# Kernel optimization log

Hardware: AMD Instinct MI355X
Metric: run time of the kernel (lower is better)

Reference implementation:

```python
import jax, jax.numpy as jnp
import numpy as np

L, B, P, D, H, DH, KV, M, S, A = 12, 8, 800, 1024, 8, 256, 1, 4096, 50, 32
ROPE_BASE = 10000.0
NEG = -1e30


def _rms(x, w):
    return (x * jax.lax.rsqrt(jnp.mean(x * x, -1, keepdims=True) + 1e-6)) * (1.0 + w)


def _rope(x, cos, sin):
    # x: [B,h,S,DH]; cos/sin: [B,1,S,DH//2]
    x1, x2 = jnp.split(x, 2, axis=-1)
    return jnp.concatenate([x1 * cos - x2 * sin, x2 * cos + x1 * sin], -1)


def setup_inputs() -> dict:
    key = jax.random.key(0)
    ks = iter(jax.random.split(key, 40))
    def nrm(shape, s=0.02):
        return jax.random.normal(next(ks), shape, jnp.float32) * s
    return {
        'prefix_pad_masks': jnp.ones((B, P), jnp.bool_),
        'x_t': jax.random.normal(next(ks), (B, S, A), jnp.float32),
        'timestep': jax.random.uniform(next(ks), (B,), jnp.float32),
        'dt': jnp.full((1,), 0.1, jnp.float32),
        'cache_k': nrm((L, B, KV, P, DH), 1.0),
        'cache_v': nrm((L, B, KV, P, DH), 1.0),
        'w_act_in': nrm((A, D)), 'b_act_in': jnp.zeros((D,), jnp.float32),
        'w_t1': nrm((D, D)), 'b_t1': jnp.zeros((D,), jnp.float32),
        'w_t2': nrm((D, D)), 'b_t2': jnp.zeros((D,), jnp.float32),
        'ln1_w': jnp.zeros((L, D), jnp.float32),
        'ada1_w': nrm((L, D, D)),
        'ln2_w': jnp.zeros((L, D), jnp.float32),
        'wq': nrm((L, D, H * DH)), 'wk': nrm((L, D, KV * DH)),
        'wv': nrm((L, D, KV * DH)), 'wo': nrm((L, H * DH, D)),
        'wg': nrm((L, D, M)), 'wu': nrm((L, D, M)), 'wd': nrm((L, M, D)),
        'lnf_w': jnp.zeros((D,), jnp.float32), 'adaf_w': nrm((D, D)),
        'w_act_out': nrm((D, A)), 'b_act_out': jnp.zeros((A,), jnp.float32),
    }


def reference(prefix_pad_masks, x_t, timestep, dt, cache_k, cache_v,
              w_act_in, b_act_in, w_t1, b_t1, w_t2, b_t2,
              ln1_w, ada1_w, ln2_w, wq, wk, wv, wo, wg, wu, wd,
              lnf_w, adaf_w, w_act_out, b_act_out):
    b, s, _ = x_t.shape
    p = prefix_pad_masks.shape[1]
    # --- embed_suffix: action projection + sinusoidal time -> MLP -> adaRMS cond ---
    suffix = x_t @ w_act_in + b_act_in                              # [B,S,D]
    half = D // 2
    freqs = jnp.exp(-jnp.log(jnp.float32(10000.0)) * jnp.arange(half, dtype=jnp.float32) / half)
    ang = timestep[:, None] * freqs[None, :]
    temb = jnp.concatenate([jnp.sin(ang), jnp.cos(ang)], -1)        # [B,D]
    cond = jax.nn.silu(temb @ w_t1 + b_t1) @ w_t2 + b_t2            # adarms_cond [B,D]
    # --- prefix-suffix 2D attention mask (make_att_2d_masks_trt) ---
    suffix_pad = jnp.ones((b, s), jnp.int32)
    suffix_att = jnp.concatenate([jnp.ones((b, 1), jnp.int32), jnp.zeros((b, s - 1), jnp.int32)], 1)
    cums = jnp.cumsum(suffix_att, 1)
    att2d = cums[:, None, :] <= cums[:, :, None]
    pad2d = (suffix_pad[:, None, :] * suffix_pad[:, :, None]).astype(bool)
    pre2d = jnp.broadcast_to(prefix_pad_masks[:, None, :], (b, s, p))
    full = jnp.concatenate([pre2d, att2d & pad2d], 2)               # [B,S,P+S]
    bias = jnp.where(full, 0.0, NEG)[:, None, :, :].astype(jnp.float32)
    # --- position ids: prefix offset + suffix cumsum - 1 ---
    offs = jnp.sum(prefix_pad_masks.astype(jnp.int32), -1)[:, None]
    pos = offs + jnp.cumsum(suffix_pad, 1) - 1                      # [B,S]
    inv = 1.0 / (ROPE_BASE ** (jnp.arange(0, DH, 2, dtype=jnp.float32) / DH))
    rang = pos[..., None].astype(jnp.float32) * inv                 # [B,S,DH/2]
    cos = jnp.cos(rang)[:, None]
    sin = jnp.sin(rang)[:, None]
    # --- gemma expert (eager attention over KV cache + suffix) ---
    h = suffix * jnp.sqrt(jnp.float32(D))
    def layer(hc, xs):
        l1, a1, l2, Wq, Wk, Wv, Wo, Wg, Wu, Wd, ck, cv = xs
        x = _rms(hc, l1) * (1.0 + (cond @ a1)[:, None, :])
        q = (x @ Wq).reshape(b, s, H, DH).transpose(0, 2, 1, 3)
        k = (x @ Wk).reshape(b, s, KV, DH).transpose(0, 2, 1, 3)
        v = (x @ Wv).reshape(b, s, KV, DH).transpose(0, 2, 1, 3)
        q = _rope(q, cos, sin)
        k = _rope(k, cos, sin)
        kf = jnp.repeat(jnp.concatenate([ck, k], 2), H // KV, 1)    # [B,H,P+S,DH]
        vf = jnp.repeat(jnp.concatenate([cv, v], 2), H // KV, 1)
        sc = jnp.einsum('bhsd,bhtd->bhst', q, kf) / jnp.sqrt(jnp.float32(DH)) + bias
        at = jax.nn.softmax(sc, -1)
        o = jnp.einsum('bhst,bhtd->bhsd', at, vf).transpose(0, 2, 1, 3).reshape(b, s, H * DH)
        hc = hc + o @ Wo
        x2 = _rms(hc, l2)
        hc = hc + (jax.nn.gelu(x2 @ Wg, approximate=True) * (x2 @ Wu)) @ Wd
        return hc, None
    h, _ = jax.lax.scan(layer, h, (ln1_w, ada1_w, ln2_w, wq, wk, wv, wo, wg, wu, wd, cache_k, cache_v))
    hf = _rms(h, lnf_w) * (1.0 + (cond @ adaf_w)[:, None, :])
    v_t = hf[:, -S:].astype(jnp.float32) @ w_act_out + b_act_out    # action_out_proj
    return x_t + dt.reshape(1, 1, 1) * v_t                          # Euler step
```

## Files before the change

kernel.cpp:

```cpp
#include <hip/hip_runtime.h>
#include <hip/hip_bf16.h>
#include <math.h>

#define NLAYER 12
#define NB 8
#define NP 800
#define ND 1024
#define NH 8
#define NDH 256
#define NM 4096
#define NS 50
#define NA 32
#define NKEYS 850
#define KPAD 896

typedef unsigned short ushort_t;
typedef unsigned int u32;
using f32x4  = __attribute__((ext_vector_type(4))) float;
using short8 = __attribute__((ext_vector_type(8))) short;

__device__ __forceinline__ u32 pack_bf2(float lo, float hi) {
  u32 a = __float_as_uint(lo);
  u32 b = __float_as_uint(hi);
  a += 0x7fffu + ((a >> 16) & 1u);
  b += 0x7fffu + ((b >> 16) & 1u);
  return (a >> 16) | (b & 0xffff0000u);
}
__device__ __forceinline__ ushort_t bf1(float x) {
  u32 a = __float_as_uint(x);
  a += 0x7fffu + ((a >> 16) & 1u);
  return (ushort_t)(a >> 16);
}
__device__ __forceinline__ float ubf(ushort_t h) {
  return __uint_as_float(((u32)h) << 16);
}
__device__ __forceinline__ void async_cp16(const void* g, const void* l) {
  __builtin_amdgcn_global_load_lds(
      (const __attribute__((address_space(1))) u32*)g,
      (__attribute__((address_space(3))) u32*)l, 16, 0, 0);
}


__global__ void cvt_copy_kernel(const float* __restrict__ src, ushort_t* __restrict__ dst, long n) {
  long i = ((long)blockIdx.x * 256 + threadIdx.x) * 8;
  if (i >= n) return;
  const float4* s4 = reinterpret_cast<const float4*>(src + i);
  float4 a = s4[0], b = s4[1];
  *reinterpret_cast<uint4*>(dst + i) =
      make_uint4(pack_bf2(a.x, a.y), pack_bf2(a.z, a.w),
                 pack_bf2(b.x, b.y), pack_bf2(b.z, b.w));
}

template<int MODE>
__global__ __launch_bounds__(256) void transpose_cvt(
    const float* __restrict__ src, long sz, ushort_t* __restrict__ dst, long dz,
    int R, int C, int ldd, int halfOff) {
  __shared__ float Ls[64][65];
  const float* s = src + (long)blockIdx.z * sz;
  ushort_t* d    = dst + (long)blockIdx.z * dz;
  int c0 = blockIdx.x * 64, r0 = blockIdx.y * 64;
  int t = threadIdx.x;
  int rr = t >> 4;
  int cc = (t & 15) * 4;
#pragma unroll
  for (int j = 0; j < 4; ++j) {
    int rl = rr + j * 16;
    int r = r0 + rl;
    float4 v = make_float4(0.f, 0.f, 0.f, 0.f);
    if (r < R) v = *reinterpret_cast<const float4*>(s + (long)r * C + c0 + cc);
    Ls[rl][cc] = v.x; Ls[rl][cc+1] = v.y; Ls[rl][cc+2] = v.z; Ls[rl][cc+3] = v.w;
  }
  __syncthreads();
  int dr = t >> 2;
  int rc = (t & 3) * 16;
  int cg = c0 + dr;
  long orow;
  if (MODE == 0) orow = cg;
  else           orow = ((long)(cg >> 5) << 6) + (cg & 31) + halfOff;
  ushort_t* drow = d + orow * ldd + r0 + rc;
#pragma unroll
  for (int i = 0; i < 16; i += 2) {
    int sr = r0 + rc + i;
    if (sr < R) {
      u32 p = pack_bf2(Ls[rc + i][dr], Ls[rc + i + 1][dr]);
      *reinterpret_cast<u32*>(drow + i) = p;
    }
  }
}


__global__ void temb_kernel(const float* __restrict__ ts, float* __restrict__ temb) {
  int idx = blockIdx.x * 256 + threadIdx.x;
  if (idx >= NB * ND) return;
  int b = idx >> 10, d = idx & 1023;
  int i = d & 511;
  float f = __expf(-logf(10000.f) * (float)i / 512.f);
  float ang = ts[b] * f;
  temb[idx] = (d < 512) ? sinf(ang) : cosf(ang);
}

__global__ void suffix_kernel(const float* __restrict__ x_t, const float* __restrict__ w,
                              const float* __restrict__ bias, float* __restrict__ h) {
  int m = blockIdx.x;
  __shared__ float xs[NA];
  if (threadIdx.x < NA) xs[threadIdx.x] = x_t[m * NA + threadIdx.x];
  __syncthreads();
  for (int n = threadIdx.x; n < ND; n += 256) {
    float acc = bias[n];
#pragma unroll
    for (int k = 0; k < NA; ++k) acc += xs[k] * w[k * ND + n];
    h[m * ND + n] = acc * 32.0f;
  }
}

__global__ void rope_table_kernel(float* __restrict__ cosT, float* __restrict__ sinT) {
  int idx = blockIdx.x * 256 + threadIdx.x;
  if (idx >= NS * 128) return;
  int s = idx >> 7, i = idx & 127;
  float inv = __expf(-(float)(2 * i) / 256.f * logf(10000.f));
  float ang = (float)(NP + s) * inv;
  cosT[idx] = cosf(ang);
  sinT[idx] = sinf(ang);
}

__global__ void rope3_kernel(const ushort_t* __restrict__ qkv0, const ushort_t* __restrict__ qkv1,
                             const float* __restrict__ cosT, const float* __restrict__ sinT,
                             ushort_t* __restrict__ qT, ushort_t* __restrict__ k_new,
                             ushort_t* __restrict__ vT_l) {
  int idx = blockIdx.x * 256 + threadIdx.x;
  if (idx >= 400 * 10 * 128) return;
  int i = idx & 127;
  int rest = idx >> 7;
  int hh = rest % 10;
  int m = rest / 10;
  int b = m / NS, s = m % NS;
  if (hh == 9) {
    int d = i;
    long base = (long)m * 2560 + 2304;
    float v0 = ubf(qkv0[base + d])       + ubf(qkv1[base + d]);
    float v1 = ubf(qkv0[base + d + 128]) + ubf(qkv1[base + d + 128]);
    vT_l[((long)(b * 256 + d)) * KPAD + NP + s]       = bf1(v0);
    vT_l[((long)(b * 256 + d + 128)) * KPAD + NP + s] = bf1(v1);
    return;
  }
  float c = cosT[s * 128 + i], sn = sinT[s * 128 + i];
  if (hh < NH) {
    long base = (long)m * 2560 + hh * 256;
    float x1 = ubf(qkv0[base + i])       + ubf(qkv1[base + i]);
    float x2 = ubf(qkv0[base + 128 + i]) + ubf(qkv1[base + 128 + i]);
    ushort_t* dst = qT + (((long)(b * NH + hh) * NS + s) * 256);
    dst[i]       = bf1(x1 * c - x2 * sn);
    dst[128 + i] = bf1(x2 * c + x1 * sn);
  } else {
    long base = (long)m * 2560 + 2048;
    float x1 = ubf(qkv0[base + i])       + ubf(qkv1[base + i]);
    float x2 = ubf(qkv0[base + 128 + i]) + ubf(qkv1[base + 128 + i]);
    ushort_t* dst = k_new + (long)m * 256;
    dst[i]       = bf1(x1 * c - x2 * sn);
    dst[128 + i] = bf1(x2 * c + x1 * sn);
  }
}

template<bool BFOUT>
__global__ void rms_kernel(const float* __restrict__ hin, const float* __restrict__ w,
                           const float* __restrict__ ada, void* __restrict__ outv) {
  int m = blockIdx.x;
  int b = m / NS;
  int d0 = threadIdx.x * 4;
  float4 v = *reinterpret_cast<const float4*>(hin + (long)m * ND + d0);
  float ss = v.x*v.x + v.y*v.y + v.z*v.z + v.w*v.w;
#pragma unroll
  for (int off = 32; off > 0; off >>= 1) ss += __shfl_down(ss, off);
  __shared__ float red[4];
  int lane = threadIdx.x & 63, wid = threadIdx.x >> 6;
  if (lane == 0) red[wid] = ss;
  __syncthreads();
  float tot = red[0] + red[1] + red[2] + red[3];
  float r = rsqrtf(tot * (1.f / ND) + 1e-6f);
  float4 wv = *reinterpret_cast<const float4*>(w + d0);
  float4 o;
  o.x = v.x * r * (1.f + wv.x);
  o.y = v.y * r * (1.f + wv.y);
  o.z = v.z * r * (1.f + wv.z);
  o.w = v.w * r * (1.f + wv.w);
  if (ada) {
    float4 av = *reinterpret_cast<const float4*>(ada + (long)b * ND + d0);
    o.x *= (1.f + av.x); o.y *= (1.f + av.y); o.z *= (1.f + av.z); o.w *= (1.f + av.w);
  }
  if (BFOUT) {
    *reinterpret_cast<uint2*>((ushort_t*)outv + (long)m * ND + d0) =
        make_uint2(pack_bf2(o.x, o.y), pack_bf2(o.z, o.w));
  } else {
    *reinterpret_cast<float4*>((float*)outv + (long)m * ND + d0) = o;
  }
}

__global__ void softmax_kernel(const float* __restrict__ sc, ushort_t* __restrict__ P) {
  int row = blockIdx.x;
  const float* p = sc + (long)row * KPAD;
  ushort_t* o = P + (long)row * KPAD;
  __shared__ float e[NKEYS];
  __shared__ float red[4];
  int lane = threadIdx.x & 63, wid = threadIdx.x >> 6;
  float mx = -1e30f;
  for (int t = threadIdx.x; t < NKEYS; t += 256) { float v = p[t]; e[t] = v; mx = fmaxf(mx, v); }
#pragma unroll
  for (int off = 32; off > 0; off >>= 1) mx = fmaxf(mx, __shfl_down(mx, off));
  if (lane == 0) red[wid] = mx;
  __syncthreads();
  mx = fmaxf(fmaxf(red[0], red[1]), fmaxf(red[2], red[3]));
  __syncthreads();
  float sum = 0.f;
  for (int t = threadIdx.x; t < NKEYS; t += 256) {
    float v = __expf(e[t] - mx);
    e[t] = v;
    sum += v;
  }
#pragma unroll
  for (int off = 32; off > 0; off >>= 1) sum += __shfl_down(sum, off);
  if (lane == 0) red[wid] = sum;
  __syncthreads();
  float inv = 1.f / (red[0] + red[1] + red[2] + red[3]);
  for (int t = threadIdx.x; t < KPAD; t += 256)
    o[t] = (t < NKEYS) ? bf1(e[t] * inv) : (ushort_t)0;
}

__global__ void final_kernel(const float* __restrict__ hf, const float* __restrict__ w,
                             const float* __restrict__ bias, const float* __restrict__ x_t,
                             const float* __restrict__ dt, float* __restrict__ out) {
  int m = blockIdx.x;
  int a = threadIdx.x & 31;
  int kg = threadIdx.x >> 5;
  float acc = 0.f;
  for (int k = kg; k < ND; k += 8) acc += hf[(long)m * ND + k] * w[k * NA + a];
  __shared__ float red[256];
  red[threadIdx.x] = acc;
  __syncthreads();
  if (threadIdx.x < NA) {
    float s = 0.f;
#pragma unroll
    for (int g = 0; g < 8; ++g) s += red[g * 32 + a];
    out[m * NA + a] = x_t[m * NA + a] + dt[0] * (s + bias[a]);
  }
}

template<int EPI, bool SPL, bool SPLITK>
__global__ __launch_bounds__(256) void gemm64(
    const ushort_t* __restrict__ A, long az,
    const ushort_t* __restrict__ B1, long b1z,
    const ushort_t* __restrict__ B2, long b2z, int nsplit, int nlim2,
    void* __restrict__ Cv, long cz,
    int M, int N, int K, int lda, int ldb, int ldc,
    float scale, int kpb, const ushort_t* __restrict__ zpad) {
  int z = blockIdx.z;
  int chunk = 0;
  int kbeg = 0, kend = K;
  if (SPLITK) { chunk = z; kbeg = z * kpb; kend = kbeg + kpb; z = 0; }
  const ushort_t* Ab  = A  + (long)z * az;
  const ushort_t* B1b = B1 + (long)z * b1z;
  const ushort_t* B2b = SPL ? (B2 + (long)z * b2z) : nullptr;

  const int m0 = blockIdx.x * 64;
  const int n0 = blockIdx.y * 64;
  const int tid = threadIdx.x;
  const int lane = tid & 63;
  const int wbase = tid & 192;
  const int wid = wbase >> 6;
  const int wm = (wid >> 1) * 32;
  const int wn = (wid & 1) * 32;
  const int l15 = lane & 15;
  const int l4  = lane >> 4;

  __shared__ ushort_t As[2][64 * 64];
  __shared__ ushort_t Bs[2][64 * 64];

  f32x4 acc[2][2] = {};

  const int ci0 = wbase + lane;
  const int row0 = ci0 >> 3;
  const int kc0 = (ci0 & 7) << 3;
  const int ci1 = 256 + ci0;
  const int row1 = ci1 >> 3;
  const int kc1 = (ci1 & 7) << 3;
  int gra0 = m0 + row0; if (gra0 > M - 1) gra0 = M - 1;
  int gra1 = m0 + row1; if (gra1 > M - 1) gra1 = M - 1;
  const int n_0 = n0 + row0;
  const int n_1 = n0 + row1;

  auto stage = [&](int buf, int k0) {
    async_cp16(Ab + (long)gra0 * lda + k0 + kc0, (const char*)As[buf] + (wbase + lane) * 16 - lane * 16 + lane * 16);
    const ushort_t* gp0;
    const ushort_t* gp1;
    if (SPL) {
      gp0 = (n_0 < nsplit) ? B1b + (long)n_0 * ldb + k0 + kc0
          : (n_0 < nlim2)  ? B2b + (long)(n_0 - nsplit) * ldb + k0 + kc0
                           : zpad + kc0;
      gp1 = (n_1 < nsplit) ? B1b + (long)n_1 * ldb + k0 + kc1
          : (n_1 < nlim2)  ? B2b + (long)(n_1 - nsplit) * ldb + k0 + kc1
                           : zpad + kc1;
    } else {
      gp0 = B1b + (long)n_0 * ldb + k0 + kc0;
      gp1 = B1b + (long)n_1 * ldb + k0 + kc1;
    }
    async_cp16(gp0, (const char*)Bs[buf] + ci0 * 16);
    async_cp16(Ab + (long)gra1 * lda + k0 + kc1, (const char*)As[buf] + ci1 * 16);
    async_cp16(gp1, (const char*)Bs[buf] + ci1 * 16);
  };

  const int nt = (kend - kbeg) >> 6;
  stage(0, kbeg);
  __syncthreads();
  int cur = 0;
  for (int t = 0; t < nt; ++t) {
    if (t + 1 < nt) stage(cur ^ 1, kbeg + (t + 1) * 64);
    const ushort_t* Ac = As[cur];
    const ushort_t* Bc = Bs[cur];
#pragma unroll
    for (int ks = 0; ks < 2; ++ks) {
      short8 af[2], bf[2];
#pragma unroll
      for (int mi = 0; mi < 2; ++mi)
        af[mi] = *reinterpret_cast<const short8*>(&Ac[(wm + mi * 16 + l15) * 64 + ks * 32 + l4 * 8]);
#pragma unroll
      for (int ni = 0; ni < 2; ++ni)
        bf[ni] = *reinterpret_cast<const short8*>(&Bc[(wn + ni * 16 + l15) * 64 + ks * 32 + l4 * 8]);
#pragma unroll
      for (int mi = 0; mi < 2; ++mi)
#pragma unroll
        for (int ni = 0; ni < 2; ++ni)
          acc[mi][ni] = __builtin_amdgcn_mfma_f32_16x16x32_bf16(af[mi], bf[ni], acc[mi][ni], 0, 0, 0);
    }
    __syncthreads();
    cur ^= 1;
  }

#pragma unroll
  for (int mi = 0; mi < 2; ++mi) {
#pragma unroll
    for (int ni = 0; ni < 2; ++ni) {
      int col = n0 + wn + ni * 16 + l15;
      int rb  = m0 + wm + mi * 16 + l4 * 4;
      if (col >= N) continue;
#pragma unroll
      for (int r = 0; r < 4; ++r) {
        int row = rb + r;
        if (row >= M) continue;
        float v = acc[mi][ni][r];
        if (EPI == 0) {
          ((float*)Cv)[(long)z * cz + (long)row * ldc + col] = v * scale;
        } else if (EPI == 3) {
          atomicAdd(&((float*)Cv)[(long)row * ldc + col], v);
        } else if (EPI == 4) {
          int hh = row / NS;
          int s  = row - hh * NS;
          ((ushort_t*)Cv)[((long)(blockIdx.z * NS + s)) * 2048 + hh * 256 + col] = bf1(v);
        } else if (EPI == 5) {
          long slab = SPLITK ? (long)chunk : (long)z;
          ((ushort_t*)Cv)[slab * cz + (long)row * ldc + col] = bf1(v);
        }
      }
    }
  }
}

__global__ __launch_bounds__(256) void gemm64G(
    const ushort_t* __restrict__ A, const ushort_t* __restrict__ B,
    ushort_t* __restrict__ C, int M, int K, int lda, int ldb, int ldc) {
  const int m0 = blockIdx.x * 64;
  const int n0 = blockIdx.y * 64;
  const int tid = threadIdx.x;
  const int lane = tid & 63;
  const int wbase = tid & 192;
  const int wid = wbase >> 6;
  const int l15 = lane & 15;
  const int l4  = lane >> 4;

  __shared__ ushort_t As[2][64 * 64];
  __shared__ ushort_t Bs[2][64 * 64];

  f32x4 acc[4] = {};

  const int ci0 = wbase + lane;
  const int row0 = ci0 >> 3;
  const int kc0 = (ci0 & 7) << 3;
  const int ci1 = 256 + ci0;
  const int row1 = ci1 >> 3;
  const int kc1 = (ci1 & 7) << 3;
  int gra0 = m0 + row0; if (gra0 > M - 1) gra0 = M - 1;
  int gra1 = m0 + row1; if (gra1 > M - 1) gra1 = M - 1;

  auto stage = [&](int buf, int k0) {
    async_cp16(A + (long)gra0 * lda + k0 + kc0, (const char*)As[buf] + ci0 * 16);
    async_cp16(B + (long)(n0 + row0) * ldb + k0 + kc0, (const char*)Bs[buf] + ci0 * 16);
    async_cp16(A + (long)gra1 * lda + k0 + kc1, (const char*)As[buf] + ci1 * 16);
    async_cp16(B + (long)(n0 + row1) * ldb + k0 + kc1, (const char*)Bs[buf] + ci1 * 16);
  };

  const int nt = K >> 6;
  stage(0, 0);
  __syncthreads();
  int cur = 0;
  for (int t = 0; t < nt; ++t) {
    if (t + 1 < nt) stage(cur ^ 1, (t + 1) * 64);
    const ushort_t* Ac = As[cur];
    const ushort_t* Bc = Bs[cur];
#pragma unroll
    for (int ks = 0; ks < 2; ++ks) {
      short8 af = *reinterpret_cast<const short8*>(&Ac[(wid * 16 + l15) * 64 + ks * 32 + l4 * 8]);
#pragma unroll
      for (int ni = 0; ni < 4; ++ni) {
        short8 bf = *reinterpret_cast<const short8*>(&Bc[(ni * 16 + l15) * 64 + ks * 32 + l4 * 8]);
        acc[ni] = __builtin_amdgcn_mfma_f32_16x16x32_bf16(af, bf, acc[ni], 0, 0, 0);
      }
    }
    __syncthreads();
    cur ^= 1;
  }

#pragma unroll
  for (int ni = 0; ni < 2; ++ni) {
    int col = (n0 >> 1) + ni * 16 + l15;
    int rb  = m0 + wid * 16 + l4 * 4;
#pragma unroll
    for (int r = 0; r < 4; ++r) {
      int row = rb + r;
      if (row >= M) continue;
      float g = acc[ni][r];
      float u = acc[ni + 2][r];
      float inner = 0.7978845608028654f * (g + 0.044715f * g * g * g);
      float t = 0.5f * g * (1.f + tanhf(inner));
      C[(long)row * ldc + col] = bf1(t * u);
    }
  }
}

template<int EPI>
__global__ __launch_bounds__(256)
void gemm_f32_kernel(const float* __restrict__ A,
                     const float* __restrict__ B1,
                     float* __restrict__ C,
                     int M, int N, int K, int lda, int ldb, int ldc,
                     const float* __restrict__ bias) {
  const int m0 = blockIdx.x * 64;
  const int n0 = blockIdx.y * 64;
// ... 134 lines not shown
        int kga = k0 + kg * 16 + kk;
        float v0 = Bb[(long)kga * ldb + gn];
        float v1 = Bb[(long)(kga + 1) * ldb + gn];
        pk[kk >> 1] = pack_bf2(v0, v1);
      }
      *reinterpret_cast<uint4*>(&Bs[n][kg * 16])     = make_uint4(pk[0],pk[1],pk[2],pk[3]);
      *reinterpret_cast<uint4*>(&Bs[n][kg * 16 + 8]) = make_uint4(pk[4],pk[5],pk[6],pk[7]);
    }
    __syncthreads();
#pragma unroll
    for (int ks = 0; ks < 2; ++ks) {
      short8 af[2], bfr[2];
#pragma unroll
      for (int mi = 0; mi < 2; ++mi)
        af[mi] = *reinterpret_cast<const short8*>(&As[wm + mi*16 + l15][ks*32 + l4*8]);
#pragma unroll
      for (int ni = 0; ni < 2; ++ni)
        bfr[ni] = *reinterpret_cast<const short8*>(&Bs[wn + ni*16 + l15][ks*32 + l4*8]);
#pragma unroll
      for (int mi = 0; mi < 2; ++mi)
#pragma unroll
        for (int ni = 0; ni < 2; ++ni)
          acc[mi][ni] = __builtin_amdgcn_mfma_f32_16x16x32_bf16(af[mi], bfr[ni], acc[mi][ni], 0, 0, 0);
    }
    __syncthreads();
  }

#pragma unroll
  for (int mi = 0; mi < 2; ++mi) {
#pragma unroll
    for (int ni = 0; ni < 2; ++ni) {
      int col = n0 + wn + ni * 16 + l15;
      int rb  = m0 + wm + mi * 16 + l4 * 4;
#pragma unroll
      for (int r = 0; r < 4; ++r) {
        int row = rb + r;
        if (row < M && col < N)
          atomicAdd(&Cb[(long)row * ldc + col], acc[mi][ni][r]);
      }
    }
  }
}

extern "C" void kernel_launch(void* const* d_in, const int* in_sizes, int n_in,
                              void* d_out, int out_size, void* d_ws, size_t ws_size,
                              hipStream_t stream) {
  (void)in_sizes; (void)n_in; (void)out_size; (void)ws_size;
  const float* x_t      = (const float*)d_in[1];
  const float* tstep    = (const float*)d_in[2];
  const float* dtp      = (const float*)d_in[3];
  const float* cache_k  = (const float*)d_in[4];
  const float* cache_v  = (const float*)d_in[5];
  const float* w_act_in = (const float*)d_in[6];
  const float* b_act_in = (const float*)d_in[7];
  const float* w_t1     = (const float*)d_in[8];
  const float* b_t1     = (const float*)d_in[9];
  const float* w_t2     = (const float*)d_in[10];
  const float* b_t2     = (const float*)d_in[11];
  const float* ln1_w    = (const float*)d_in[12];
  const float* ada1_w   = (const float*)d_in[13];
  const float* ln2_w    = (const float*)d_in[14];
  const float* wq       = (const float*)d_in[15];
  const float* wk       = (const float*)d_in[16];
  const float* wv       = (const float*)d_in[17];
  const float* wo       = (const float*)d_in[18];
  const float* wg       = (const float*)d_in[19];
  const float* wu       = (const float*)d_in[20];
  const float* wd       = (const float*)d_in[21];
  const float* lnf_w    = (const float*)d_in[22];
  const float* adaf_w   = (const float*)d_in[23];
  const float* wao      = (const float*)d_in[24];
  const float* bao      = (const float*)d_in[25];
  float* outp = (float*)d_out;

  char* p = (char*)d_ws;
  auto alloc = [&](size_t bytes) { char* r = p; p += (bytes + 255) & ~(size_t)255; return r; };

  ushort_t* wqkvT  = (ushort_t*)alloc((size_t)12 * 2560 * 1024 * 2);
  ushort_t* woT    = (ushort_t*)alloc((size_t)12 * 1024 * 2048 * 2);
  ushort_t* wguT   = (ushort_t*)alloc((size_t)12 * 8192 * 1024 * 2);
  ushort_t* wdT    = (ushort_t*)alloc((size_t)12 * 1024 * 4096 * 2);
  ushort_t* kcache = (ushort_t*)alloc((size_t)12 * 8 * NP * 256 * 2);
  ushort_t* vT     = (ushort_t*)alloc((size_t)12 * 8 * 256 * KPAD * 2);
  ushort_t* qkvp   = (ushort_t*)alloc((size_t)2 * 400 * 2560 * 2);
  ushort_t* qT     = (ushort_t*)alloc((size_t)8 * 400 * 256 * 2);
  ushort_t* k_new  = (ushort_t*)alloc((size_t)400 * 256 * 2);
  float*    sc     = (float*)alloc((size_t)8 * 400 * KPAD * 4);
  ushort_t* P      = (ushort_t*)alloc((size_t)8 * 400 * KPAD * 2);
  ushort_t* o_buf  = (ushort_t*)alloc((size_t)400 * 2048 * 2);
  ushort_t* t_buf  = (ushort_t*)alloc((size_t)400 * 4096 * 2);
  ushort_t* x_buf  = (ushort_t*)alloc((size_t)400 * 1024 * 2);
  float*    h_buf  = (float*)alloc((size_t)400 * 1024 * 4);
  float*    hf     = (float*)alloc((size_t)400 * 1024 * 4);
  float*    temb   = (float*)alloc(8 * 1024 * 4);
  float*    tmp    = (float*)alloc(8 * 1024 * 4);
  float*    cond   = (float*)alloc(8 * 1024 * 4);
  float*    ada_all= (float*)alloc((size_t)12 * 8 * 1024 * 4);
  float*    adaf_o = (float*)alloc(8 * 1024 * 4);
  float*    cosT   = (float*)alloc(NS * 128 * 4);
  float*    sinT   = (float*)alloc(NS * 128 * 4);
  ushort_t* zpad   = (ushort_t*)alloc(512 * 2);

  hipMemsetAsync(zpad, 0, 512 * 2, stream);
  hipMemsetAsync(ada_all, 0, ((size_t)12 * 8 * 1024 + 8 * 1024) * 4, stream);

  {
    long n = (long)12 * 8 * NP * 256;
    cvt_copy_kernel<<<(int)((n / 8 + 255) / 256), 256, 0, stream>>>(cache_k, kcache, n);
  }
  transpose_cvt<0><<<dim3(32, 16, 12), 256, 0, stream>>>(wq, (long)1024 * 2048, wqkvT, (long)2560 * 1024, 1024, 2048, 1024, 0);
  transpose_cvt<0><<<dim3(4, 16, 12), 256, 0, stream>>>(wk, (long)1024 * 256, wqkvT + (long)2048 * 1024, (long)2560 * 1024, 1024, 256, 1024, 0);
  transpose_cvt<0><<<dim3(4, 16, 12), 256, 0, stream>>>(wv, (long)1024 * 256, wqkvT + (long)2304 * 1024, (long)2560 * 1024, 1024, 256, 1024, 0);
  transpose_cvt<0><<<dim3(16, 32, 12), 256, 0, stream>>>(wo, (long)2048 * 1024, woT, (long)1024 * 2048, 2048, 1024, 2048, 0);
  transpose_cvt<1><<<dim3(64, 16, 12), 256, 0, stream>>>(wg, (long)1024 * 4096, wguT, (long)8192 * 1024, 1024, 4096, 1024, 0);
  transpose_cvt<1><<<dim3(64, 16, 12), 256, 0, stream>>>(wu, (long)1024 * 4096, wguT, (long)8192 * 1024, 1024, 4096, 1024, 32);
  transpose_cvt<0><<<dim3(16, 64, 12), 256, 0, stream>>>(wd, (long)4096 * 1024, wdT, (long)1024 * 4096, 4096, 1024, 4096, 0);
  transpose_cvt<0><<<dim3(4, 13, 96), 256, 0, stream>>>(cache_v, (long)NP * 256, vT, (long)256 * KPAD, NP, 256, KPAD, 0);

  temb_kernel<<<32, 256, 0, stream>>>(tstep, temb);
  suffix_kernel<<<400, 256, 0, stream>>>(x_t, w_act_in, b_act_in, h_buf);
  rope_table_kernel<<<25, 256, 0, stream>>>(cosT, sinT);
  gemm_f32_kernel<2><<<dim3(1, 16, 1), 256, 0, stream>>>(temb, w_t1, tmp, NB, ND, ND, ND, ND, ND, b_t1);
  gemm_f32_kernel<1><<<dim3(1, 16, 1), 256, 0, stream>>>(tmp, w_t2, cond, NB, ND, ND, ND, ND, ND, b_t2);
  gemm_f32sk<<<dim3(1, 16, 48), 256, 0, stream>>>(cond, ada1_w, (long)ND * ND, ada_all, (long)NB * ND, NB, ND, ND, ND, ND, ND, 4);
  gemm_f32sk<<<dim3(1, 16, 4), 256, 0, stream>>>(cond, adaf_w, 0, adaf_o, 0, NB, ND, ND, ND, ND, ND, 4);

  for (int l = 0; l < NLAYER; ++l) {
    rms_kernel<true><<<400, 256, 0, stream>>>(h_buf, ln1_w + (long)l * ND, ada_all + (long)l * NB * ND, x_buf);
    gemm64<5, false, true><<<dim3(7, 40, 2), 256, 0, stream>>>(
        x_buf, 0, wqkvT + (long)l * 2560 * 1024, 0, nullptr, 0, 0, 0,
        qkvp, (long)400 * 2560, 400, 2560, 1024, 1024, 1024, 2560, 1.f, 512, zpad);
    rope3_kernel<<<2000, 256, 0, stream>>>(qkvp, qkvp + (long)400 * 2560, cosT, sinT,
                                           qT, k_new, vT + (long)l * 8 * 256 * KPAD);
    gemm64<0, true, false><<<dim3(7, 14, 8), 256, 0, stream>>>(
        qT, (long)400 * 256,
        kcache + (long)l * 8 * NP * 256, (long)NP * 256,
        k_new, (long)NS * 256, NP, NKEYS,
        sc, (long)400 * KPAD, 400, KPAD, 256, 256, 256, KPAD, 0.0625f, 0, zpad);
    softmax_kernel<<<3200, 256, 0, stream>>>(sc, P);
    gemm64<4, false, false><<<dim3(7, 4, 8), 256, 0, stream>>>(
        P, (long)400 * KPAD,
        vT + (long)l * 8 * 256 * KPAD, (long)256 * KPAD, nullptr, 0, 0, 0,
        o_buf, 0, 400, 256, KPAD, KPAD, KPAD, 2048, 1.f, 0, zpad);
    gemm64<3, false, true><<<dim3(7, 16, 4), 256, 0, stream>>>(
        o_buf, 0, woT + (long)l * 1024 * 2048, 0, nullptr, 0, 0, 0,
        h_buf, 0, 400, 1024, 2048, 2048, 2048, 1024, 1.f, 512, zpad);
    rms_kernel<true><<<400, 256, 0, stream>>>(h_buf, ln2_w + (long)l * ND, nullptr, x_buf);
    gemm64G<<<dim3(7, 128, 1), 256, 0, stream>>>(
        x_buf, wguT + (long)l * 8192 * 1024, t_buf, 400, 1024, 1024, 1024, 4096);
    gemm64<3, false, true><<<dim3(7, 16, 4), 256, 0, stream>>>(
        t_buf, 0, wdT + (long)l * 1024 * 4096, 0, nullptr, 0, 0, 0,
        h_buf, 0, 400, 1024, 4096, 4096, 4096, 1024, 1.f, 1024, zpad);
  }

  rms_kernel<false><<<400, 256, 0, stream>>>(h_buf, lnf_w, adaf_o, hf);
  final_kernel<<<400, 256, 0, stream>>>(hf, wao, bao, x_t, dtp, outp);
}
```

Measured before the change: 2.049 ms.

## Fuse RoPE into QKV GEMM and replace attention with split-K flash kernel

Interleaves the rotary halves in the Q/K weight and K-cache layouts so the QKV GEMM epilogue can apply RoPE with a lane shuffle. This removes the split-K partial buffer and the separate rope kernel. Attention's score GEMM, softmax and PV GEMM are replaced by a flash-style kernel that splits keys into 128-key chunks, followed by a combine kernel that merges the per-chunk max and sum. The score and probability matrices no longer go through global memory, at the cost of fp32 partial outputs per chunk and an extra combine pass. The QKV GEMM also drops its split-K, which halves its grid parallelism.

```diff
diff --git a/kernel.cpp b/kernel.cpp
--- a/kernel.cpp
+++ b/kernel.cpp
@@ -13,6 +13,7 @@
 #define NA 32
 #define NKEYS 850
 #define KPAD 896
+#define CH 128
 
 typedef unsigned short ushort_t;
 typedef unsigned int u32;
@@ -41,14 +42,18 @@
 }
 
 
-__global__ void cvt_copy_kernel(const float* __restrict__ src, ushort_t* __restrict__ dst, long n) {
-  long i = ((long)blockIdx.x * 256 + threadIdx.x) * 8;
-  if (i >= n) return;
-  const float4* s4 = reinterpret_cast<const float4*>(src + i);
-  float4 a = s4[0], b = s4[1];
-  *reinterpret_cast<uint4*>(dst + i) =
-      make_uint4(pack_bf2(a.x, a.y), pack_bf2(a.z, a.w),
-                 pack_bf2(b.x, b.y), pack_bf2(b.z, b.w));
+__global__ void cvt_permute_kernel(const float* __restrict__ src, ushort_t* __restrict__ dst, long nrows) {
+  long idx = (long)blockIdx.x * 256 + threadIdx.x;
+  long row = idx >> 5;
+  int t = (int)(idx & 31);
+  if (row >= nrows) return;
+  const float* s = src + row * 256 + t * 4;
+  float4 lo = *reinterpret_cast<const float4*>(s);
+  float4 hi = *reinterpret_cast<const float4*>(s + 128);
+  ushort_t* d = dst + row * 256 + t * 8;
+  *reinterpret_cast<uint4*>(d) =
+      make_uint4(pack_bf2(lo.x, hi.x), pack_bf2(lo.y, hi.y),
+                 pack_bf2(lo.z, hi.z), pack_bf2(lo.w, hi.w));
 }
 
 template<int MODE>
@@ -75,8 +80,9 @@
   int rc = (t & 3) * 16;
   int cg = c0 + dr;
   long orow;
-  if (MODE == 0) orow = cg;
-  else           orow = ((long)(cg >> 5) << 6) + (cg & 31) + halfOff;
+  if (MODE == 0)      orow = cg;
+  else if (MODE == 1) orow = ((long)(cg >> 5) << 6) + (cg & 31) + halfOff;
+  else                orow = (long)(cg & ~255) + ((cg & 127) << 1) + ((cg >> 7) & 1);
   ushort_t* drow = d + orow * ldd + r0 + rc;
 #pragma unroll
   for (int i = 0; i < 16; i += 2) {
@@ -121,44 +127,6 @@
   float ang = (float)(NP + s) * inv;
   cosT[idx] = cosf(ang);
   sinT[idx] = sinf(ang);
-}
-
-__global__ void rope3_kernel(const ushort_t* __restrict__ qkv0, const ushort_t* __restrict__ qkv1,
-                             const float* __restrict__ cosT, const float* __restrict__ sinT,
-                             ushort_t* __restrict__ qT, ushort_t* __restrict__ k_new,
-                             ushort_t* __restrict__ vT_l) {
-  int idx = blockIdx.x * 256 + threadIdx.x;
-  if (idx >= 400 * 10 * 128) return;
-  int i = idx & 127;
-  int rest = idx >> 7;
-  int hh = rest % 10;
-  int m = rest / 10;
-  int b = m / NS, s = m % NS;
-  if (hh == 9) {
-    int d = i;
-    long base = (long)m * 2560 + 2304;
-    float v0 = ubf(qkv0[base + d])       + ubf(qkv1[base + d]);
-    float v1 = ubf(qkv0[base + d + 128]) + ubf(qkv1[base + d + 128]);
-    vT_l[((long)(b * 256 + d)) * KPAD + NP + s]       = bf1(v0);
-    vT_l[((long)(b * 256 + d + 128)) * KPAD + NP + s] = bf1(v1);
-    return;
-  }
-  float c = cosT[s * 128 + i], sn = sinT[s * 128 + i];
-  if (hh < NH) {
-    long base = (long)m * 2560 + hh * 256;
-    float x1 = ubf(qkv0[base + i])       + ubf(qkv1[base + i]);
-    float x2 = ubf(qkv0[base + 128 + i]) + ubf(qkv1[base + 128 + i]);
-    ushort_t* dst = qT + (((long)(b * NH + hh) * NS + s) * 256);
-    dst[i]       = bf1(x1 * c - x2 * sn);
-    dst[128 + i] = bf1(x2 * c + x1 * sn);
-  } else {
-    long base = (long)m * 2560 + 2048;
-    float x1 = ubf(qkv0[base + i])       + ubf(qkv1[base + i]);
-    float x2 = ubf(qkv0[base + 128 + i]) + ubf(qkv1[base + 128 + i]);
-    ushort_t* dst = k_new + (long)m * 256;
-    dst[i]       = bf1(x1 * c - x2 * sn);
-    dst[128 + i] = bf1(x2 * c + x1 * sn);
-  }
 }
 
 template<bool BFOUT>
@@ -195,36 +163,6 @@
   }
 }
 
-__global__ void softmax_kernel(const float* __restrict__ sc, ushort_t* __restrict__ P) {
-  int row = blockIdx.x;
-  const float* p = sc + (long)row * KPAD;
-  ushort_t* o = P + (long)row * KPAD;
-  __shared__ float e[NKEYS];
-  __shared__ float red[4];
-  int lane = threadIdx.x & 63, wid = threadIdx.x >> 6;
-  float mx = -1e30f;
-  for (int t = threadIdx.x; t < NKEYS; t += 256) { float v = p[t]; e[t] = v; mx = fmaxf(mx, v); }
-#pragma unroll
-  for (int off = 32; off > 0; off >>= 1) mx = fmaxf(mx, __shfl_down(mx, off));
-  if (lane == 0) red[wid] = mx;
-  __syncthreads();
-  mx = fmaxf(fmaxf(red[0], red[1]), fmaxf(red[2], red[3]));
-  __syncthreads();
-  float sum = 0.f;
-  for (int t = threadIdx.x; t < NKEYS; t += 256) {
-    float v = __expf(e[t] - mx);
-    e[t] = v;
-    sum += v;
-  }
-#pragma unroll
-  for (int off = 32; off > 0; off >>= 1) sum += __shfl_down(sum, off);
-  if (lane == 0) red[wid] = sum;
-  __syncthreads();
-  float inv = 1.f / (red[0] + red[1] + red[2] + red[3]);
-  for (int t = threadIdx.x; t < KPAD; t += 256)
-    o[t] = (t < NKEYS) ? bf1(e[t] * inv) : (ushort_t)0;
-}
-
 __global__ void final_kernel(const float* __restrict__ hf, const float* __restrict__ w,
                              const float* __restrict__ bias, const float* __restrict__ x_t,
                              const float* __restrict__ dt, float* __restrict__ out) {
@@ -244,21 +182,13 @@
   }
 }
 
-template<int EPI, bool SPL, bool SPLITK>
-__global__ __launch_bounds__(256) void gemm64(
-    const ushort_t* __restrict__ A, long az,
-    const ushort_t* __restrict__ B1, long b1z,
-    const ushort_t* __restrict__ B2, long b2z, int nsplit, int nlim2,
-    void* __restrict__ Cv, long cz,
-    int M, int N, int K, int lda, int ldb, int ldc,
-    float scale, int kpb, const ushort_t* __restrict__ zpad) {
-  int z = blockIdx.z;
-  int chunk = 0;
-  int kbeg = 0, kend = K;
-  if (SPLITK) { chunk = z; kbeg = z * kpb; kend = kbeg + kpb; z = 0; }
-  const ushort_t* Ab  = A  + (long)z * az;
-  const ushort_t* B1b = B1 + (long)z * b1z;
-  const ushort_t* B2b = SPL ? (B2 + (long)z * b2z) : nullptr;
+__global__ __launch_bounds__(256) void gemm64acc(
+    const ushort_t* __restrict__ A,
+    const ushort_t* __restrict__ B,
+    float* __restrict__ C,
+    int M, int N, int K, int lda, int ldb, int ldc, int kpb) {
+  const int kbeg = blockIdx.z * kpb;
+  const int kend = kbeg + kpb;
 
   const int m0 = blockIdx.x * 64;
   const int n0 = blockIdx.y * 64;
@@ -288,23 +218,10 @@
   const int n_1 = n0 + row1;
 
   auto stage = [&](int buf, int k0) {
-    async_cp16(Ab + (long)gra0 * lda + k0 + kc0, (const char*)As[buf] + (wbase + lane) * 16 - lane * 16 + lane * 16);
-    const ushort_t* gp0;
-    const ushort_t* gp1;
-    if (SPL) {
-      gp0 = (n_0 < nsplit) ? B1b + (long)n_0 * ldb + k0 + kc0
-          : (n_0 < nlim2)  ? B2b + (long)(n_0 - nsplit) * ldb + k0 + kc0
-                           : zpad + kc0;
-      gp1 = (n_1 < nsplit) ? B1b + (long)n_1 * ldb + k0 + kc1
-          : (n_1 < nlim2)  ? B2b + (long)(n_1 - nsplit) * ldb + k0 + kc1
-                           : zpad + kc1;
-    } else {
-      gp0 = B1b + (long)n_0 * ldb + k0 + kc0;
-      gp1 = B1b + (long)n_1 * ldb + k0 + kc1;
-    }
-    async_cp16(gp0, (const char*)Bs[buf] + ci0 * 16);
-    async_cp16(Ab + (long)gra1 * lda + k0 + kc1, (const char*)As[buf] + ci1 * 16);
-    async_cp16(gp1, (const char*)Bs[buf] + ci1 * 16);
+    async_cp16(A + (long)gra0 * lda + k0 + kc0, (const char*)As[buf] + ci0 * 16);
+    async_cp16(B + (long)n_0 * ldb + k0 + kc0, (const char*)Bs[buf] + ci0 * 16);
+    async_cp16(A + (long)gra1 * lda + k0 + kc1, (const char*)As[buf] + ci1 * 16);
+    async_cp16(B + (long)n_1 * ldb + k0 + kc1, (const char*)Bs[buf] + ci1 * 16);
   };
 
   const int nt = (kend - kbeg) >> 6;
@@ -345,21 +262,324 @@
       for (int r = 0; r < 4; ++r) {
         int row = rb + r;
         if (row >= M) continue;
+        atomicAdd(&C[(long)row * ldc + col], acc[mi][ni][r]);
+      }
+    }
+  }
+}
+
+__global__ __launch_bounds__(256) void gemm64rope(
+    const ushort_t* __restrict__ A,
+    const ushort_t* __restrict__ B,
+    const float* __restrict__ cosT, const float* __restrict__ sinT,
+    ushort_t* __restrict__ qTo, ushort_t* __restrict__ k_new,
+    ushort_t* __restrict__ vT_l) {
+  const int M = 400, K = 1024, lda = 1024, ldb = 1024;
+  const int m0 = blockIdx.x * 64;
+  const int n0 = blockIdx.y * 64;
+  const int tid = threadIdx.x;
+  const int lane = tid & 63;
+  const int wbase = tid & 192;
+  const int wid = wbase >> 6;
+  const int wm = (wid >> 1) * 32;
+  const int wn = (wid & 1) * 32;
+  const int l15 = lane & 15;
+  const int l4  = lane >> 4;
+
+  __shared__ ushort_t As[2][64 * 64];
+  __shared__ ushort_t Bs[2][64 * 64];
+
+  f32x4 acc[2][2] = {};
+
+  const int ci0 = wbase + lane;
+  const int row0 = ci0 >> 3;
+  const int kc0 = (ci0 & 7) << 3;
+  const int ci1 = 256 + ci0;
+  const int row1 = ci1 >> 3;
+  const int kc1 = (ci1 & 7) << 3;
+  int gra0 = m0 + row0; if (gra0 > M - 1) gra0 = M - 1;
+  int gra1 = m0 + row1; if (gra1 > M - 1) gra1 = M - 1;
+  const int n_0 = n0 + row0;
+  const int n_1 = n0 + row1;
+
+  auto stage = [&](int buf, int k0) {
+    async_cp16(A + (long)gra0 * lda + k0 + kc0, (const char*)As[buf] + ci0 * 16);
+    async_cp16(B + (long)n_0 * ldb + k0 + kc0, (const char*)Bs[buf] + ci0 * 16);
+    async_cp16(A + (long)gra1 * lda + k0 + kc1, (const char*)As[buf] + ci1 * 16);
+    async_cp16(B + (long)n_1 * ldb + k0 + kc1, (const char*)Bs[buf] + ci1 * 16);
+  };
+
+  stage(0, 0);
+  __syncthreads();
+  int cur = 0;
+  for (int t = 0; t < 16; ++t) {
+    if (t + 1 < 16) stage(cur ^ 1, (t + 1) * 64);
+    const ushort_t* Ac = As[cur];
+    const ushort_t* Bc = Bs[cur];
+#pragma unroll
+    for (int ks = 0; ks < 2; ++ks) {
+      short8 af[2], bf[2];
+#pragma unroll
+      for (int mi = 0; mi < 2; ++mi)
+        af[mi] = *reinterpret_cast<const short8*>(&Ac[(wm + mi * 16 + l15) * 64 + ks * 32 + l4 * 8]);
+#pragma unroll
+      for (int ni = 0; ni < 2; ++ni)
+        bf[ni] = *reinterpret_cast<const short8*>(&Bc[(wn + ni * 16 + l15) * 64 + ks * 32 + l4 * 8]);
+#pragma unroll
+      for (int mi = 0; mi < 2; ++mi)
+#pragma unroll
+        for (int ni = 0; ni < 2; ++ni)
+          acc[mi][ni] = __builtin_amdgcn_mfma_f32_16x16x32_bf16(af[mi], bf[ni], acc[mi][ni], 0, 0, 0);
+    }
+    __syncthreads();
+    cur ^= 1;
+  }
+
+#pragma unroll
+  for (int mi = 0; mi < 2; ++mi) {
+#pragma unroll
+    for (int ni = 0; ni < 2; ++ni) {
+      int col = n0 + wn + ni * 16 + l15;
+      int rb  = m0 + wm + mi * 16 + l4 * 4;
+      float pv[4];
+#pragma unroll
+      for (int r = 0; r < 4; ++r) pv[r] = __shfl_xor(acc[mi][ni][r], 1);
+#pragma unroll
+      for (int r = 0; r < 4; ++r) {
+        int row = rb + r;
+        if (row >= 400) continue;
+        int b = row / NS, s = row - b * NS;
         float v = acc[mi][ni][r];
-        if (EPI == 0) {
-          ((float*)Cv)[(long)z * cz + (long)row * ldc + col] = v * scale;
-        } else if (EPI == 3) {
-          atomicAdd(&((float*)Cv)[(long)row * ldc + col], v);
-        } else if (EPI == 4) {
-          int hh = row / NS;
-          int s  = row - hh * NS;
-          ((ushort_t*)Cv)[((long)(blockIdx.z * NS + s)) * 2048 + hh * 256 + col] = bf1(v);
-        } else if (EPI == 5) {
-          long slab = SPLITK ? (long)chunk : (long)z;
-          ((ushort_t*)Cv)[slab * cz + (long)row * ldc + col] = bf1(v);
+        if (col < 2304) {
+          int j = col & 255;
+          int i = j >> 1;
+          float c = cosT[s * 128 + i], sn = sinT[s * 128 + i];
+          float o = (col & 1) ? (v * c + pv[r] * sn) : (v * c - pv[r] * sn);
+          if (col < 2048)
+            qTo[((long)((b << 3) + (col >> 8)) * NS + s) * 256 + j] = bf1(o);
+          else
+            k_new[(long)row * 256 + j] = bf1(o);
+        } else {
+          vT_l[((long)(b * 256 + (col - 2304))) * KPAD + NP + s] = bf1(v);
         }
       }
     }
+  }
+}
+
+__global__ __launch_bounds__(256) void flash_kernel(
+    const ushort_t* __restrict__ qT,
+    const ushort_t* __restrict__ kcache_l,
+    const ushort_t* __restrict__ k_new,
+    const ushort_t* __restrict__ vT_l,
+    const ushort_t* __restrict__ zpad,
+    float* __restrict__ opart, float* __restrict__ mpart, float* __restrict__ lpart) {
+  const int bh = blockIdx.x;
+  const int ch = blockIdx.y;
+  const int b  = bh >> 3;
+  const int tid = threadIdx.x;
+  const int lane = tid & 63;
+  const int w = tid >> 6;
+  const int wm = (w >> 1) * 32;
+  const int wns = (w & 1) * 64;
+  const int l15 = lane & 15;
+  const int l4  = lane >> 4;
+
+  __shared__ __align__(16) char lds[66560];
+  ushort_t* Qs = (ushort_t*)lds;
+  ushort_t* Ks = (ushort_t*)(lds + 32768);
+  ushort_t* Ps = (ushort_t*)(lds + 49152);
+  float* SMm = (float*)(lds + 65536);
+  float* SMl = (float*)(lds + 66048);
+  ushort_t* Vs = (ushort_t*)lds;
+
+#pragma unroll
+  for (int i = 0; i < 8; ++i) {
+    int ci = i * 256 + tid;
+    int qrow = ci >> 5; int seg = ci & 31;
+    int qr = qrow < NS ? qrow : NS - 1;
+    async_cp16(qT + ((long)bh * NS + qr) * 256 + seg * 8, (char*)Qs + ci * 16);
+  }
+
+  f32x4 s2[2][4] = {};
+  for (int kk = 0; kk < 4; ++kk) {
+#pragma unroll
+    for (int i = 0; i < 4; ++i) {
+      int ci = i * 256 + tid;
+      int krow = ci >> 3; int seg = ci & 7;
+      int key = ch * CH + krow;
+      const ushort_t* src;
+      if (key < NP)         src = kcache_l + ((long)(b * NP + key)) * 256 + kk * 64 + seg * 8;
+      else if (key < NKEYS) src = k_new + ((long)(b * NS + key - NP)) * 256 + kk * 64 + seg * 8;
+      else                  src = zpad + seg * 8;
+      async_cp16(src, (char*)Ks + ci * 16);
+    }
+    __syncthreads();
+#pragma unroll
+    for (int ks = 0; ks < 2; ++ks) {
+      short8 af[2], bf[4];
+#pragma unroll
+      for (int mi = 0; mi < 2; ++mi)
+        af[mi] = *reinterpret_cast<const short8*>(&Qs[(wm + mi * 16 + l15) * 256 + kk * 64 + ks * 32 + l4 * 8]);
+#pragma unroll
+      for (int ni = 0; ni < 4; ++ni)
+        bf[ni] = *reinterpret_cast<const short8*>(&Ks[(wns + ni * 16 + l15) * 64 + ks * 32 + l4 * 8]);
+#pragma unroll
+      for (int mi = 0; mi < 2; ++mi)
+#pragma unroll
+        for (int ni = 0; ni < 4; ++ni)
+          s2[mi][ni] = __builtin_amdgcn_mfma_f32_16x16x32_bf16(af[mi], bf[ni], s2[mi][ni], 0, 0, 0);
+    }
+    __syncthreads();
+  }
+
+  float mx[2][4];
+#pragma unroll
+  for (int mi = 0; mi < 2; ++mi)
+#pragma unroll
+    for (int r = 0; r < 4; ++r) mx[mi][r] = -1e30f;
+#pragma unroll
+  for (int mi = 0; mi < 2; ++mi)
+#pragma unroll
+    for (int ni = 0; ni < 4; ++ni) {
+      int key = ch * CH + wns + ni * 16 + l15;
+      bool valid = key < NKEYS;
+#pragma unroll
+      for (int r = 0; r < 4; ++r) {
+        float v = s2[mi][ni][r] * 0.0625f;
+        v = valid ? v : -1e30f;
+        s2[mi][ni][r] = v;
+        mx[mi][r] = fmaxf(mx[mi][r], v);
+      }
+    }
+#pragma unroll
+  for (int off = 1; off < 16; off <<= 1)
+#pragma unroll
+    for (int mi = 0; mi < 2; ++mi)
+#pragma unroll
+      for (int r = 0; r < 4; ++r)
+        mx[mi][r] = fmaxf(mx[mi][r], __shfl_xor(mx[mi][r], off));
+  if (l15 == 0) {
+#pragma unroll
+    for (int mi = 0; mi < 2; ++mi)
+#pragma unroll
+      for (int r = 0; r < 4; ++r)
+        SMm[(w & 1) * 64 + wm + mi * 16 + l4 * 4 + r] = mx[mi][r];
+  }
+  __syncthreads();
+  float mrow[2][4], sum[2][4];
+#pragma unroll
+  for (int mi = 0; mi < 2; ++mi)
+#pragma unroll
+    for (int r = 0; r < 4; ++r) {
+      int row = wm + mi * 16 + l4 * 4 + r;
+      mrow[mi][r] = fmaxf(SMm[row], SMm[64 + row]);
+      sum[mi][r] = 0.f;
+    }
+#pragma unroll
+  for (int mi = 0; mi < 2; ++mi)
+#pragma unroll
+    for (int ni = 0; ni < 4; ++ni) {
+      int colp = wns + ni * 16 + l15;
+#pragma unroll
+      for (int r = 0; r < 4; ++r) {
+        float e = __expf(s2[mi][ni][r] - mrow[mi][r]);
+        Ps[(wm + mi * 16 + l4 * 4 + r) * 128 + colp] = bf1(e);
+        sum[mi][r] += e;
+      }
+    }
+#pragma unroll
+  for (int off = 1; off < 16; off <<= 1)
+#pragma unroll
+    for (int mi = 0; mi < 2; ++mi)
+#pragma unroll
+      for (int r = 0; r < 4; ++r)
+        sum[mi][r] += __shfl_xor(sum[mi][r], off);
+  if (l15 == 0) {
+#pragma unroll
+    for (int mi = 0; mi < 2; ++mi)
+#pragma unroll
+      for (int r = 0; r < 4; ++r)
+        SMl[(w & 1) * 64 + wm + mi * 16 + l4 * 4 + r] = sum[mi][r];
+  }
+  __syncthreads();
+  if ((w & 1) == 0 && l15 == 0) {
+#pragma unroll
+    for (int mi = 0; mi < 2; ++mi)
+#pragma unroll
+      for (int r = 0; r < 4; ++r) {
+        int row = wm + mi * 16 + l4 * 4 + r;
+        if (row < NS) {
+          mpart[((long)bh * 7 + ch) * NS + row] = mrow[mi][r];
+          lpart[((long)bh * 7 + ch) * NS + row] = SMl[row] + SMl[64 + row];
+        }
+      }
+  }
+
+  f32x4 o2[2][8] = {};
+  for (int kk = 0; kk < 2; ++kk) {
+#pragma unroll
+    for (int i = 0; i < 8; ++i) {
+      int ci = i * 256 + tid;
+      int vd = ci >> 3; int seg = ci & 7;
+      async_cp16(vT_l + ((long)(b * 256 + vd)) * KPAD + ch * CH + kk * 64 + seg * 8,
+                 (char*)Vs + ci * 16);
+    }
+    __syncthreads();
+#pragma unroll
+    for (int ks = 0; ks < 2; ++ks) {
+      short8 af[2], bf[8];
+#pragma unroll
+      for (int mi = 0; mi < 2; ++mi)
+        af[mi] = *reinterpret_cast<const short8*>(&Ps[(wm + mi * 16 + l15) * 128 + kk * 64 + ks * 32 + l4 * 8]);
+#pragma unroll
+      for (int ni = 0; ni < 8; ++ni)
+        bf[ni] = *reinterpret_cast<const short8*>(&Vs[((w & 1) * 128 + ni * 16 + l15) * 64 + ks * 32 + l4 * 8]);
+#pragma unroll
+      for (int mi = 0; mi < 2; ++mi)
+#pragma unroll
+        for (int ni = 0; ni < 8; ++ni)
+          o2[mi][ni] = __builtin_amdgcn_mfma_f32_16x16x32_bf16(af[mi], bf[ni], o2[mi][ni], 0, 0, 0);
+    }
+    __syncthreads();
+  }
+
+#pragma unroll
+  for (int mi = 0; mi < 2; ++mi)
+#pragma unroll
+    for (int ni = 0; ni < 8; ++ni) {
+      int col = (w & 1) * 128 + ni * 16 + l15;
+#pragma unroll
+      for (int r = 0; r < 4; ++r) {
+        int row = wm + mi * 16 + l4 * 4 + r;
+        if (row < NS)
+          opart[(((long)bh * 7 + ch) * NS + row) * 256 + col] = o2[mi][ni][r];
+      }
+    }
+}
+
+__global__ void att_combine(const float* __restrict__ opart, const float* __restrict__ mpart,
+                            const float* __restrict__ lpart, ushort_t* __restrict__ o_buf) {
+  int blk = blockIdx.x;
+  int b = blk / NS, s = blk - b * NS;
+  int d = threadIdx.x;
+  for (int h = 0; h < NH; ++h) {
+    int bh = b * NH + h;
+    float mv[7];
+    float m = -1e30f;
+#pragma unroll
+    for (int c = 0; c < 7; ++c) {
+      mv[c] = mpart[((long)bh * 7 + c) * NS + s];
+      m = fmaxf(m, mv[c]);
+    }
+    float den = 0.f, o = 0.f;
+#pragma unroll
+    for (int c = 0; c < 7; ++c) {
+      float wgt = __expf(mv[c] - m);
+      den += wgt * lpart[((long)bh * 7 + c) * NS + s];
+      o   += wgt * opart[(((long)bh * 7 + c) * NS + s) * 256 + d];
+    }
+    o_buf[(long)blk * 2048 + h * 256 + d] = bf1(o / den);
   }
 }
 
@@ -660,11 +880,11 @@
   ushort_t* wdT    = (ushort_t*)alloc((size_t)12 * 1024 * 4096 * 2);
   ushort_t* kcache = (ushort_t*)alloc((size_t)12 * 8 * NP * 256 * 2);
   ushort_t* vT     = (ushort_t*)alloc((size_t)12 * 8 * 256 * KPAD * 2);
-  ushort_t* qkvp   = (ushort_t*)alloc((size_t)2 * 400 * 2560 * 2);
-  ushort_t* qT     = (ushort_t*)alloc((size_t)8 * 400 * 256 * 2);
+  ushort_t* qT     = (ushort_t*)alloc((size_t)64 * NS * 256 * 2);
   ushort_t* k_new  = (ushort_t*)alloc((size_t)400 * 256 * 2);
-  float*    sc     = (float*)alloc((size_t)8 * 400 * KPAD * 4);
-  ushort_t* P      = (ushort_t*)alloc((size_t)8 * 400 * KPAD * 2);
+  float*    opart  = (float*)alloc((size_t)64 * 7 * NS * 256 * 4);
+  float*    mpart  = (float*)alloc((size_t)64 * 7 * NS * 4);
+  float*    lpart  = (float*)alloc((size_t)64 * 7 * NS * 4);
   ushort_t* o_buf  = (ushort_t*)alloc((size_t)400 * 2048 * 2);
   ushort_t* t_buf  = (ushort_t*)alloc((size_t)400 * 4096 * 2);
   ushort_t* x_buf  = (ushort_t*)alloc((size_t)400 * 1024 * 2);
@@ -682,12 +902,9 @@
   hipMemsetAsync(zpad, 0, 512 * 2, stream);
   hipMemsetAsync(ada_all, 0, ((size_t)12 * 8 * 1024 + 8 * 1024) * 4, stream);
 
-  {
-    long n = (long)12 * 8 * NP * 256;
-    cvt_copy_kernel<<<(int)((n / 8 + 255) / 256), 256, 0, stream>>>(cache_k, kcache, n);
-  }
-  transpose_cvt<0><<<dim3(32, 16, 12), 256, 0, stream>>>(wq, (long)1024 * 2048, wqkvT, (long)2560 * 1024, 1024, 2048, 1024, 0);
-  transpose_cvt<0><<<dim3(4, 16, 12), 256, 0, stream>>>(wk, (long)1024 * 256, wqkvT + (long)2048 * 1024, (long)2560 * 1024, 1024, 256, 1024, 0);
+  cvt_permute_kernel<<<9600, 256, 0, stream>>>(cache_k, kcache, (long)12 * 8 * NP);
+  transpose_cvt<2><<<dim3(32, 16, 12), 256, 0, stream>>>(wq, (long)1024 * 2048, wqkvT, (long)2560 * 1024, 1024, 2048, 1024, 0);
+  transpose_cvt<2><<<dim3(4, 16, 12), 256, 0, stream>>>(wk, (long)1024 * 256, wqkvT + (long)2048 * 1024, (long)2560 * 1024, 1024, 256, 1024, 0);
   transpose_cvt<0><<<dim3(4, 16, 12), 256, 0, stream>>>(wv, (long)1024 * 256, wqkvT + (long)2304 * 1024, (long)2560 * 1024, 1024, 256, 1024, 0);
   transpose_cvt<0><<<dim3(16, 32, 12), 256, 0, stream>>>(wo, (long)2048 * 1024, woT, (long)1024 * 2048, 2048, 1024, 2048, 0);
   transpose_cvt<1><<<dim3(64, 16, 12), 256, 0, stream>>>(wg, (long)1024 * 4096, wguT, (long)8192 * 1024, 1024, 4096, 1024, 0);
@@ -704,31 +921,20 @@
   gemm_f32sk<<<dim3(1, 16, 4), 256, 0, stream>>>(cond, adaf_w, 0, adaf_o, 0, NB, ND, ND, ND, ND, ND, 4);
 
   for (int l = 0; l < NLAYER; ++l) {
+    ushort_t* vT_l = vT + (long)l * 8 * 256 * KPAD;
     rms_kernel<true><<<400, 256, 0, stream>>>(h_buf, ln1_w + (long)l * ND, ada_all + (long)l * NB * ND, x_buf);
-    gemm64<5, false, true><<<dim3(7, 40, 2), 256, 0, stream>>>(
-        x_buf, 0, wqkvT + (long)l * 2560 * 1024, 0, nullptr, 0, 0, 0,
-        qkvp, (long)400 * 2560, 400, 2560, 1024, 1024, 1024, 2560, 1.f, 512, zpad);
-    rope3_kernel<<<2000, 256, 0, stream>>>(qkvp, qkvp + (long)400 * 2560, cosT, sinT,
-                                           qT, k_new, vT + (long)l * 8 * 256 * KPAD);
-    gemm64<0, true, false><<<dim3(7, 14, 8), 256, 0, stream>>>(
-        qT, (long)400 * 256,
-        kcache + (long)l * 8 * NP * 256, (long)NP * 256,
-        k_new, (long)NS * 256, NP, NKEYS,
-        sc, (long)400 * KPAD, 400, KPAD, 256, 256, 256, KPAD, 0.0625f, 0, zpad);
-    softmax_kernel<<<3200, 256, 0, stream>>>(sc, P);
-    gemm64<4, false, false><<<dim3(7, 4, 8), 256, 0, stream>>>(
-        P, (long)400 * KPAD,
-        vT + (long)l * 8 * 256 * KPAD, (long)256 * KPAD, nullptr, 0, 0, 0,
-        o_buf, 0, 400, 256, KPAD, KPAD, KPAD, 2048, 1.f, 0, zpad);
-    gemm64<3, false, true><<<dim3(7, 16, 4), 256, 0, stream>>>(
-        o_buf, 0, woT + (long)l * 1024 * 2048, 0, nullptr, 0, 0, 0,
-        h_buf, 0, 400, 1024, 2048, 2048, 2048, 1024, 1.f, 512, zpad);
+    gemm64rope<<<dim3(7, 40, 1), 256, 0, stream>>>(
+        x_buf, wqkvT + (long)l * 2560 * 1024, cosT, sinT, qT, k_new, vT_l);
+    flash_kernel<<<dim3(64, 7, 1), 256, 0, stream>>>(
+        qT, kcache + (long)l * 8 * NP * 256, k_new, vT_l, zpad, opart, mpart, lpart);
+    att_combine<<<400, 256, 0, stream>>>(opart, mpart, lpart, o_buf);
+    gemm64acc<<<dim3(7, 16, 4), 256, 0, stream>>>(
+        o_buf, woT + (long)l * 1024 * 2048, h_buf, 400, 1024, 2048, 2048, 2048, 1024, 512);
     rms_kernel<true><<<400, 256, 0, stream>>>(h_buf, ln2_w + (long)l * ND, nullptr, x_buf);
     gemm64G<<<dim3(7, 128, 1), 256, 0, stream>>>(
         x_buf, wguT + (long)l * 8192 * 1024, t_buf, 400, 1024, 1024, 1024, 4096);
-    gemm64<3, false, true><<<dim3(7, 16, 4), 256, 0, stream>>>(
-        t_buf, 0, wdT + (long)l * 1024 * 4096, 0, nullptr, 0, 0, 0,
-        h_buf, 0, 400, 1024, 4096, 4096, 4096, 1024, 1.f, 1024, zpad);
+    gemm64acc<<<dim3(7, 16, 4), 256, 0, stream>>>(
+        t_buf, wdT + (long)l * 1024 * 4096, h_buf, 400, 1024, 4096, 4096, 4096, 1024, 1024);
   }
 
   rms_kernel<false><<<400, 256, 0, stream>>>(h_buf, lnf_w, adaf_o, hf);
```

Result: no change. 2.042 ms (-0.3%).
